# Performance work log

Hardware: AMD Instinct MI355X
Metric: run time of the kernel (lower is better)

## Reference

```python
import jax, jax.numpy as jnp
import numpy as np

B, N, P, E = 64, 512, 256, 4096          # batch, nodes (stations), partition nodes, edges
NUM_NWP, LP, F = 8, 16, 32               # num_nwp, local_points, local_cnn_dims
NT, ED, H, W = 8, 8, 64, 8               # num_temp, edge_feature_dims, decf_mlp_hidden, weight_function_dim
G, RH = 64, 256                          # gnn_dim, readout_hid_dim
H1, Q = 128, 9                           # mlp_hid_dim1, num quantiles


def setup_inputs() -> dict:
    key = jax.random.key(0)
    ks = iter(jax.random.split(key, 40))
    def rn(shape, s=0.05):
        return jax.random.normal(next(ks), shape, dtype=jnp.float32) * s
    # one-hot incidence matrices: each edge has one left (partition) node and one right node
    lidx = jax.random.randint(next(ks), (E,), 0, P)
    ridx = jax.random.randint(next(ks), (E,), 0, N)
    linc = jnp.zeros((P, E), jnp.float32).at[lidx, jnp.arange(E)].set(1.0)
    rinc = jnp.zeros((E, N), jnp.float32).at[jnp.arange(E), ridx].set(1.0)
    inp = {
        "x1": jax.random.normal(next(ks), (B, NUM_NWP * N, LP), dtype=jnp.float32),
        "x2": jax.random.normal(next(ks), (B, NT), dtype=jnp.float32),
        # LocalConv1D grouped conv (torch OIW layout: [Cout, Cin/groups, K])
        "conv_w": rn((F * N, NUM_NWP, LP)), "conv_b": rn((F * N,)),
        # WDSGCN2 edge-weight MLP
        "k1_w": rn((H, ED)), "k1_b": rn((H,)),
        "k2_w": rn((H, NT)),
        "k3_w": rn((H, F)),
        "k4_w": rn((H, F)),
        "k5_w": rn((W, H)), "k5_b": rn((W,)),
        "gc_w": rn((G, F * W)), "gc_b": rn((G,)),
        # readout
        "r0_w": rn((RH, G * P)),
        "r1_w": rn((RH, NT)), "r1_b": rn((RH,)),
        "r2_w": rn((RH, P)),
        "r3_w": rn((P, RH)), "r3_b": rn((P,)),
        # SMlp (forward uses l1 -> ELU -> l3 only)
        "l1_w": rn((H1, NT + G)), "l1_b": rn((H1,)),
        "l3_w": rn((Q, H1)), "l3_b": rn((Q,)),
        # buffers
        "ef": jax.random.normal(next(ks), (E, ED + 1), dtype=jnp.float32),
        "linc": linc,
        "rinc": rinc,
        "cap_feature": jax.random.normal(next(ks), (P,), dtype=jnp.float32),
        "partition_idx": jnp.arange(P, dtype=jnp.int32) * (N // P),
    }
    return inp


def reference(x1, x2, conv_w, conv_b, k1_w, k1_b, k2_w, k3_w, k4_w, k5_w, k5_b,
              gc_w, gc_b, r0_w, r1_w, r1_b, r2_w, r3_w, r3_b,
              l1_w, l1_b, l3_w, l3_b, ef, linc, rinc, cap_feature, partition_idx):
    b = x1.shape[0]
    # --- LocalConv1D: grouped conv1d (valid padding, output length 1) + ReLU ---
    y = jax.lax.conv_general_dilated(x1, conv_w, (1,), 'VALID',
                                     dimension_numbers=('NCH', 'OIH', 'NCH'),
                                     feature_group_count=N)
    x = jax.nn.relu(y + conv_b[None, :, None]).reshape(b, N, F)      # [B,N,F]
    # --- WDSGCN2: per-edge weight kernel ---
    kern = ef[:, :-1] @ k1_w.T + k1_b                                # [E,H]
    kern = kern[None] + (x2 @ k2_w.T)[:, None, :]                    # [B,E,H]
    xp = x[:, partition_idx, :]                                      # [B,P,F]
    kern = kern + jnp.einsum('pe,bpf->bef', linc, xp) @ k3_w.T       # left-node feats
    rx = jnp.einsum('en,bnf->bef', rinc, x)                          # right-node feats [B,E,F]
    kern = kern + rx @ k4_w.T
    kern = jax.nn.relu(jax.nn.leaky_relu(kern, 0.02) @ k5_w.T + k5_b)  # [B,E,W]
    # --- message = kernel (outer) right-node features, aggregated by left incidence ---
    msg = kern[:, :, :, None] * rx[:, :, None, :]                    # [B,E,W,F]
    agg = jnp.einsum('pe,bewf->bpwf', linc, msg).reshape(b, P, W * F)
    yg = jax.nn.relu(agg @ gc_w.T + gc_b)                            # [B,P,G]
    # --- readout attention over partition nodes ---
    h = yg.reshape(b, -1) @ r0_w.T + (x2 @ r1_w.T + r1_b) + cap_feature @ r2_w.T
    wt = jax.nn.relu(jax.nn.leaky_relu(h, 0.01) @ r3_w.T + r3_b)     # [B,P]
    res = jnp.einsum('bp,bpg->bg', wt, yg)                           # [B,G]
    # --- SMlp head ---
    z = jnp.concatenate([res, x2], axis=1)
    z = jax.nn.elu(z @ l1_w.T + l1_b)
    return z @ l3_w.T + l3_b                                         # [B,Q]
```

## Files before the change

kernel.cpp:

```cpp
#include <hip/hip_runtime.h>
#include <math.h>

#define B_ 64
#define N_ 512
#define P_ 256
#define E_ 4096
#define F_ 32
#define H_ 64
#define W_ 8
#define G_ 64
#define RH_ 256

#define X_OFF   0
#define T4_OFF  (X_OFF + N_*B_*F_)
#define T3_OFF  (T4_OFF + N_*B_*H_)
#define KB_OFF  (T3_OFF + P_*B_*H_)
#define KW_OFF  (KB_OFF + E_*H_)
#define YG_OFF  (KW_OFF + E_*B_*W_)
#define HB_OFF  (YG_OFF + B_*P_*G_)
#define RES_OFF (HB_OFF + B_*RH_)
#define INT_OFF (RES_OFF + 4*B_*G_)

__global__ __launch_bounds__(256) void k_decode(const float* __restrict__ linc,
    const float* __restrict__ rinc, int* __restrict__ lidx, int* __restrict__ ridx) {
  int i4 = blockIdx.x * 256 + threadIdx.x;
  const int L4 = (P_ * E_) / 4;
  if (i4 < L4) {
    float4 v = ((const float4*)linc)[i4];
    int i = i4 * 4;
    int p = i >> 12, e = i & 4095;
    if (v.x != 0.0f) lidx[e]     = p;
    if (v.y != 0.0f) lidx[e + 1] = p;
    if (v.z != 0.0f) lidx[e + 2] = p;
    if (v.w != 0.0f) lidx[e + 3] = p;
  } else {
    int j4 = i4 - L4;
    float4 v = ((const float4*)rinc)[j4];
    int j = j4 * 4;
    int e = j >> 9, n = j & 511;
    if (v.x != 0.0f) ridx[e] = n;
    if (v.y != 0.0f) ridx[e] = n + 1;
    if (v.z != 0.0f) ridx[e] = n + 2;
    if (v.w != 0.0f) ridx[e] = n + 3;
  }
}

__global__ __launch_bounds__(1024) void k_lists(const int* __restrict__ lidx,
    int* __restrict__ part_start, int* __restrict__ part_edges) {
  __shared__ int cnt[256];
  __shared__ int buf[256];
  __shared__ int cur[256];
  int t = threadIdx.x;
  if (t < 256) cnt[t] = 0;
  __syncthreads();
  for (int e = t; e < E_; e += 1024) atomicAdd(&cnt[lidx[e]], 1);
  __syncthreads();
  if (t < 256) buf[t] = cnt[t];
  __syncthreads();
  for (int off = 1; off < 256; off <<= 1) {
    int add = 0;
    if (t < 256 && t >= off) add = buf[t - off];
    __syncthreads();
    if (t < 256) buf[t] += add;
    __syncthreads();
  }
  if (t < 256) {
    part_start[t + 1] = buf[t];
    if (t == 0) part_start[0] = 0;
    cur[t] = buf[t] - cnt[t];
  }
  __syncthreads();
  for (int e = t; e < E_; e += 1024) {
    int p = lidx[e];
    int pos = atomicAdd(&cur[p], 1);
    part_edges[pos] = e;
  }
}

__global__ __launch_bounds__(256) void k_conv(const float* __restrict__ x1,
    const float* __restrict__ conv_w, const float* __restrict__ conv_b,
    float* __restrict__ x) {
  __shared__ float wsm[32 * 132];
  __shared__ float xsm[8192];
  int n = blockIdx.x, t = threadIdx.x;
  for (int i = t; i < 1024; i += 256) {
    int f = i >> 5, j = i & 31;
    ((float4*)wsm)[f * 33 + j] = ((const float4*)(conv_w + n * 4096))[i];
  }
  for (int i = t; i < 2048; i += 256) {
    int b = i >> 5, j = i & 31;
    ((float4*)xsm)[i] = ((const float4*)(x1 + b * 65536 + n * 128))[j];
  }
  __syncthreads();
  int f = t & 31, bq = t >> 5;
  float cb = conv_b[n * 32 + f];
  float acc[8];
#pragma unroll
  for (int bi = 0; bi < 8; bi++) acc[bi] = cb;
  const float4* wf4 = (const float4*)wsm + f * 33;
  const float4* xb4 = (const float4*)xsm + bq * 256;
#pragma unroll 4
  for (int k4 = 0; k4 < 32; k4++) {
    float4 wv = wf4[k4];
#pragma unroll
    for (int bi = 0; bi < 8; bi++) {
      float4 xv = xb4[bi * 32 + k4];
      acc[bi] += wv.x * xv.x + wv.y * xv.y + wv.z * xv.z + wv.w * xv.w;
    }
  }
#pragma unroll
  for (int bi = 0; bi < 8; bi++) {
    int b = bq * 8 + bi;
    x[n * 2048 + b * 32 + f] = fmaxf(acc[bi], 0.0f);
  }
}

__global__ __launch_bounds__(256) void k_prep(
    const float* __restrict__ x, const int* __restrict__ pidx,
    const float* __restrict__ k3_w, const float* __restrict__ k4_w,
    const float* __restrict__ x2, const float* __restrict__ k2_w,
    const float* __restrict__ ef, const float* __restrict__ k1_w,
    const float* __restrict__ k1_b,
    const float* __restrict__ r1_w, const float* __restrict__ r1_b,
    const float* __restrict__ r2_w, const float* __restrict__ cap,
    float* __restrict__ t4, float* __restrict__ t3, float* __restrict__ kb,
    float* __restrict__ hbuf) {
  __shared__ float xsh[2048];
  __shared__ float wsh[64 * 36];
  __shared__ float x2s[512];
  __shared__ float k2s[512];
  int blk = blockIdx.x, t = threadIdx.x;
  if (blk < 768) {
    bool isT4 = blk < 512;
    int n = isT4 ? blk : pidx[blk - 512];
    const float* wmat = isT4 ? k4_w : k3_w;
    float* outp = isT4 ? (t4 + blk * 4096) : (t3 + (blk - 512) * 4096);
    for (int i = t; i < 512; i += 256) {
      ((float4*)xsh)[i] = ((const float4*)(x + n * 2048))[i];
      int h = i >> 3, j = i & 7;
      ((float4*)wsh)[h * 9 + j] = ((const float4*)wmat)[i];
    }
    if (isT4) {
      for (int i = t; i < 128; i += 256) {
        ((float4*)x2s)[i] = ((const float4*)x2)[i];
        ((float4*)k2s)[i] = ((const float4*)k2_w)[i];
      }
    }
    __syncthreads();
    int h = t & 63, bq = t >> 6;
    float wreg[32];
#pragma unroll
    for (int j = 0; j < 8; j++) {
      float4 v = ((float4*)wsh)[h * 9 + j];
      wreg[4 * j] = v.x; wreg[4 * j + 1] = v.y; wreg[4 * j + 2] = v.z; wreg[4 * j + 3] = v.w;
    }
    float w2[8];
    if (isT4) {
      float4 u = ((float4*)k2s)[h * 2], v = ((float4*)k2s)[h * 2 + 1];
      w2[0] = u.x; w2[1] = u.y; w2[2] = u.z; w2[3] = u.w;
      w2[4] = v.x; w2[5] = v.y; w2[6] = v.z; w2[7] = v.w;
    }
    for (int bi = 0; bi < 16; bi++) {
      int b = bq * 16 + bi;
      float acc = 0.0f;
#pragma unroll
      for (int j = 0; j < 8; j++) {
        float4 xv = ((float4*)xsh)[b * 8 + j];
        acc += xv.x * wreg[4 * j] + xv.y * wreg[4 * j + 1] +
               xv.z * wreg[4 * j + 2] + xv.w * wreg[4 * j + 3];
      }
      if (isT4) {
        float4 u = ((float4*)x2s)[b * 2], v = ((float4*)x2s)[b * 2 + 1];
        acc += u.x * w2[0] + u.y * w2[1] + u.z * w2[2] + u.w * w2[3] +
               v.x * w2[4] + v.y * w2[5] + v.z * w2[6] + v.w * w2[7];
      }
      outp[b * 64 + h] = acc;
    }
  } else if (blk < 1792) {
    int o = (blk - 768) * 256 + t;
    int e = o >> 6, h = o & 63;
    float acc = k1_b[h];
    const float* er = ef + e * 9;
    const float* kr = k1_w + h * 8;
#pragma unroll
    for (int d = 0; d < 8; d++) acc += er[d] * kr[d];
    kb[o] = acc;
  } else {
    int o = (blk - 1792) * 256 + t;
    int rh = o & 255;
    float acc = r1_b[rh];
    const float* xr = x2 + (o >> 8) * 8;
    const float* rr = r1_w + rh * 8;
#pragma unroll
    for (int d = 0; d < 8; d++) acc += xr[d] * rr[d];
    const float* r2r = r2_w + rh * 256;
    for (int p4 = 0; p4 < 64; p4++) {
      float4 cv = ((const float4*)cap)[p4];
      float4 rv = ((const float4*)r2r)[p4];
      acc += cv.x * rv.x + cv.y * rv.y + cv.z * rv.z + cv.w * rv.w;
    }
    hbuf[o] = acc;
  }
}

__global__ __launch_bounds__(256) void k_edge(
    const float* __restrict__ kb, const float* __restrict__ t3,
    const float* __restrict__ t4, const float* __restrict__ k5_w,
    const float* __restrict__ k5_b, const int* __restrict__ lidx,
    const int* __restrict__ ridx, float* __restrict__ kw) {
  __shared__ float k5t[4 * 520];
  int e = blockIdx.x, t = threadIdx.x;
  for (int i = t; i < 512; i += 256) {
    int h = i >> 3, w = i & 7;
    float v = k5_w[w * 64 + h];
#pragma unroll
    for (int qq = 0; qq < 4; qq++) k5t[qq * 520 + i] = v;
  }
  int p = lidx[e], r = ridx[e];
  int q = t & 3, b = t >> 2;
  const float4* kb4 = (const float4*)(kb + e * 64 + q * 16);
  const float4* t34 = (const float4*)(t3 + p * 4096 + b * 64 + q * 16);
  const float4* t44 = (const float4*)(t4 + r * 4096 + b * 64 + q * 16);
  __syncthreads();
  float lk[16];
#pragma unroll
  for (int j4 = 0; j4 < 4; j4++) {
    float4 a = kb4[j4], c = t34[j4], d = t44[j4];
    float v;
    v = a.x + c.x + d.x; lk[j4 * 4 + 0] = v > 0.0f ? v : 0.02f * v;
    v = a.y + c.y + d.y; lk[j4 * 4 + 1] = v > 0.0f ? v : 0.02f * v;
    v = a.z + c.z + d.z; lk[j4 * 4 + 2] = v > 0.0f ? v : 0.02f * v;
    v = a.w + c.w + d.w; lk[j4 * 4 + 3] = v > 0.0f ? v : 0.02f * v;
  }
  float pw[8] = {0, 0, 0, 0, 0, 0, 0, 0};
  const float* kq = k5t + q * 520 + q * 128;
#pragma unroll
  for (int j = 0; j < 16; j++) {
    float4 u = *(const float4*)(kq + j * 8);
    float4 v = *(const float4*)(kq + j * 8 + 4);
    float l = lk[j];
    pw[0] += l * u.x; pw[1] += l * u.y; pw[2] += l * u.z; pw[3] += l * u.w;
    pw[4] += l * v.x; pw[5] += l * v.y; pw[6] += l * v.z; pw[7] += l * v.w;
  }
#pragma unroll
  for (int w = 0; w < 8; w++) {
    pw[w] += __shfl_xor(pw[w], 1);
    pw[w] += __shfl_xor(pw[w], 2);
  }
  float2 o;
  o.x = fmaxf(pw[2 * q] + k5_b[2 * q], 0.0f);
  o.y = fmaxf(pw[2 * q + 1] + k5_b[2 * q + 1], 0.0f);
  *(float2*)(kw + e * 512 + t * 2) = o;
}

__global__ __launch_bounds__(256) void k_agg_gc(const float* __restrict__ x,
    const float* __restrict__ kw, const int* __restrict__ ridx,
    const int* __restrict__ part_start, const int* __restrict__ part_edges,
    const float* __restrict__ gc_w, const float* __restrict__ gc_b,
    float* __restrict__ yg) {
  __shared__ unsigned short accS[64 * 256];
  int p = blockIdx.x, t = threadIdx.x;
  int b = t >> 2, s = t & 3;
  float acc[64];
#pragma unroll
  for (int j = 0; j < 64; j++) acc[j] = 0.0f;
  int s0 = part_start[p], s1 = part_start[p + 1];
  int idx = s0;
  for (; idx + 1 < s1; idx += 2) {
    int e0 = part_edges[idx], e1 = part_edges[idx + 1];
    int r0 = ridx[e0], r1 = ridx[e1];
    float2 ka = *(const float2*)(kw + e0 * 512 + b * 8 + s * 2);
    float2 kc = *(const float2*)(kw + e1 * 512 + b * 8 + s * 2);
    const float4* xp0 = (const float4*)(x + r0 * 2048 + b * 32);
    const float4* xp1 = (const float4*)(x + r1 * 2048 + b * 32);
    float xa[32], xb[32];
#pragma unroll
    for (int i = 0; i < 8; i++) {
      float4 v = xp0[i];
      xa[4 * i] = v.x; xa[4 * i + 1] = v.y; xa[4 * i + 2] = v.z; xa[4 * i + 3] = v.w;
    }
#pragma unroll
    for (int i = 0; i < 8; i++) {
      float4 v = xp1[i];
      xb[4 * i] = v.x; xb[4 * i + 1] = v.y; xb[4 * i + 2] = v.z; xb[4 * i + 3] = v.w;
    }
#pragma unroll
    for (int j = 0; j < 32; j++) acc[j] += ka.x * xa[j];
#pragma unroll
    for (int j = 0; j < 32; j++) acc[32 + j] += ka.y * xa[j];
#pragma unroll
    for (int j = 0; j < 32; j++) acc[j] += kc.x * xb[j];
#pragma unroll
    for (int j = 0; j < 32; j++) acc[32 + j] += kc.y * xb[j];
  }
  if (idx < s1) {
    int e0 = part_edges[idx];
    int r0 = ridx[e0];
    float2 ka = *(const float2*)(kw + e0 * 512 + b * 8 + s * 2);
    const float4* xp0 = (const float4*)(x + r0 * 2048 + b * 32);
    float xa[32];
#pragma unroll
    for (int i = 0; i < 8; i++) {
      float4 v = xp0[i];
      xa[4 * i] = v.x; xa[4 * i + 1] = v.y; xa[4 * i + 2] = v.z; xa[4 * i + 3] = v.w;
    }
#pragma unroll
    for (int j = 0; j < 32; j++) acc[j] += ka.x * xa[j];
#pragma unroll
    for (int j = 0; j < 32; j++) acc[32 + j] += ka.y * xa[j];
  }
#pragma unroll
  for (int o = 0; o < 8; o++) {
    int koct = s * 8 + o;
    int os = koct ^ (b >> 3);
    unsigned int wds[4];
#pragma unroll
    for (int h = 0; h < 4; h++) {
      unsigned int u0 = __float_as_uint(acc[o * 8 + 2 * h]);
      u0 = u0 + 0x7fffu + ((u0 >> 16) & 1u);
      unsigned int u1 = __float_as_uint(acc[o * 8 + 2 * h + 1]);
      u1 = u1 + 0x7fffu + ((u1 >> 16) & 1u);
      wds[h] = (u0 >> 16) | (u1 & 0xffff0000u);
    }
    int4 pk = make_int4((int)wds[0], (int)wds[1], (int)wds[2], (int)wds[3]);
    *(int4*)(accS + b * 256 + os * 8) = pk;
  }
  __syncthreads();
  int lane = t & 63, wv = t >> 6;
  int bg = lane >> 3, gg = lane & 7;
  int g0 = wv * 16 + gg * 2;
  const float* gw0 = gc_w + g0 * 256;
  const float* gw1 = gc_w + (g0 + 1) * 256;
  float ac[8][2];
#pragma unroll
  for (int i = 0; i < 8; i++) { ac[i][0] = 0.0f; ac[i][1] = 0.0f; }
  for (int oct = 0; oct < 32; oct++) {
    int4 a8[8];
#pragma unroll
    for (int i = 0; i < 8; i++) {
      int row = bg * 8 + i;
      int os = oct ^ bg;
      a8[i] = *(const int4*)(accS + row * 256 + os * 8);
    }
    float4 b0a = *(const float4*)(gw0 + oct * 8);
    float4 b0b = *(const float4*)(gw0 + oct * 8 + 4);
    float4 b1a = *(const float4*)(gw1 + oct * 8);
    float4 b1b = *(const float4*)(gw1 + oct * 8 + 4);
    float bv0[8] = {b0a.x, b0a.y, b0a.z, b0a.w, b0b.x, b0b.y, b0b.z, b0b.w};
    float bv1[8] = {b1a.x, b1a.y, b1a.z, b1a.w, b1b.x, b1b.y, b1b.z, b1b.w};
#pragma unroll
    for (int kk = 0; kk < 8; kk++) {
#pragma unroll
      for (int i = 0; i < 8; i++) {
        int w32;
        switch (kk >> 1) {
          case 0: w32 = a8[i].x; break;
          case 1: w32 = a8[i].y; break;
          case 2: w32 = a8[i].z; break;
          default: w32 = a8[i].w; break;
        }
        unsigned int u = (unsigned int)w32;
        unsigned int bits = (kk & 1) ? (u & 0xffff0000u) : (u << 16);
        float av = __uint_as_float(bits);
        ac[i][0] += av * bv0[kk];
        ac[i][1] += av * bv1[kk];
      }
    }
  }
  float gb0 = gc_b[g0], gb1 = gc_b[g0 + 1];
#pragma unroll
  for (int i = 0; i < 8; i++) {
    int bb = bg * 8 + i;
    float* yp = yg + bb * 16384 + p * 64;
    yp[g0]     = fmaxf(ac[i][0] + gb0, 0.0f);
    yp[g0 + 1] = fmaxf(ac[i][1] + gb1, 0.0f);
  }
}

__global__ __launch_bounds__(256) void k_r0(const float* __restrict__ yg,
    const float* __restrict__ r0_w, float* __restrict__ hbuf) {
  __shared__ float ygs[64 * 68];
  __shared__ float r0s[32 * 68];
  int blk = blockIdx.x;
  int rt = blk >> 6, kc = blk & 63;
  int t = threadIdx.x;
  int bg = t & 15, rg = t >> 4;
  float acc[4][2];
#pragma unroll
  for (int bi = 0; bi < 4; bi++)
#pragma unroll
    for (int ri = 0; ri < 2; ri++) acc[bi][ri] = 0.0f;
  for (int ks = 0; ks < 4; ks++) {
    int kbase = kc * 256 + ks * 64;
    __syncthreads();
    for (int i = t; i < 1024; i += 256) {
      int b = i >> 4, j = i & 15;
      ((float4*)ygs)[b * 17 + j] = *((const float4*)(yg + b * 16384 + kbase) + j);
    }
    for (int i = t; i < 512; i += 256) {
      int r = i >> 4, j = i & 15;
      ((float4*)r0s)[r * 17 + j] = *((const float4*)(r0_w + (rt * 32 + r) * 16384 + kbase) + j);
    }
    __syncthreads();
#pragma unroll 4
    for (int k4 = 0; k4 < 16; k4++) {
      float4 yv[4], rv[2];
#pragma unroll
      for (int bi = 0; bi < 4; bi++) yv[bi] = ((float4*)ygs)[(bg * 4 + bi) * 17 + k4];
#pragma unroll
      for (int ri = 0; ri < 2; ri++) rv[ri] = ((float4*)r0s)[(rg * 2 + ri) * 17 + k4];
#pragma unroll
      for (int bi = 0; bi < 4; bi++)
#pragma unroll
        for (int ri = 0; ri < 2; ri++)
          acc[bi][ri] += yv[bi].x * rv[ri].x + yv[bi].y * rv[ri].y +
                         yv[bi].z * rv[ri].z + yv[bi].w * rv[ri].w;
    }
  }
#pragma unroll
  for (int bi = 0; bi < 4; bi++)
#pragma unroll
    for (int ri = 0; ri < 2; ri++)
      atomicAdd(&hbuf[(bg * 4 + bi) * 256 + rt * 32 + rg * 2 + ri], acc[bi][ri]);
}

__global__ __launch_bounds__(256) void k_wt_res(const float* __restrict__ hbuf,
    const float* __restrict__ r3_w, const float* __restrict__ r3_b,
    const float* __restrict__ yg, float* __restrict__ res4) {
  __shared__ float hs[256];
  __shared__ float wts[64];
  __shared__ float red[256];
  int blk = blockIdx.x;
  int bb = blk >> 2, pq = blk & 3;
  int t = threadIdx.x;
  float hv = hbuf[bb * 256 + t];
  hs[t] = hv > 0.0f ? hv : 0.01f * hv;
  __syncthreads();
  int pl = t >> 2, c = t & 3;
  int pp = pq * 64 + pl;
  const float4* wrow = (const float4*)(r3_w + pp * 256 + c * 64);
  const float4* h4 = (const float4*)(hs) + c * 16;
  float a = 0.0f;
#pragma unroll
  for (int j = 0; j < 16; j++) {
    float4 w4 = wrow[j], hh = h4[j];
    a += hh.x * w4.x + hh.y * w4.y + hh.z * w4.z + hh.w * w4.w;
  }
  a += __shfl_xor(a, 1);
  a += __shfl_xor(a, 2);
  if (c == 0) wts[pl] = fmaxf(a + r3_b[pp], 0.0f);
  __syncthreads();
  int g = t & 63, ch = t >> 6;
  float r = 0.0f;
  const float* ygp = yg + bb * 16384 + pq * 4096 + g;
#pragma unroll
  for (int pi = 0; pi < 16; pi++) {
    int pl2 = ch * 16 + pi;
    r += wts[pl2] * ygp[pl2 * 64];
  }
  red[t] = r;
  __syncthreads();
  if (t < 64)
    res4[pq * 4096 + bb * 64 + t] = red[t] + red[t + 64] + red[t + 128] + red[t + 192];
}

__global__ __launch_bounds__(128) void k_final(const float* __restrict__ res4,
    const float* __restrict__ x2, const float* __restrict__ l1_w,
    const float* __restrict__ l1_b, const float* __restrict__ l3_w,
    const float* __restrict__ l3_b, float* __restrict__ out) {
  __shared__ float zs[128];
  int bb = blockIdx.x, t = threadIdx.x;
  float acc = l1_b[t];
  const float* wrow = l1_w + t * 72;
  const float* rr = res4 + bb * 64;
#pragma unroll 8
  for (int j = 0; j < 64; j++) {
    float rv = rr[j] + rr[4096 + j] + rr[8192 + j] + rr[12288 + j];
    acc += rv * wrow[j];
  }
  const float* xr = x2 + bb * 8;
#pragma unroll
  for (int j = 0; j < 8; j++) acc += xr[j] * wrow[64 + j];
  zs[t] = acc > 0.0f ? acc : expm1f(acc);
  __syncthreads();
  if (t < 9) {
    float o = l3_b[t];
    const float* w3 = l3_w + t * 128;
    for (int j = 0; j < 128; j++) o += zs[j] * w3[j];
    out[bb * 9 + t] = o;
  }
}

extern "C" void kernel_launch(void* const* d_in, const int* in_sizes, int n_in,
                              void* d_out, int out_size, void* d_ws, size_t ws_size,
                              hipStream_t stream) {
  (void)in_sizes; (void)n_in; (void)out_size; (void)ws_size;
  const float* x1     = (const float*)d_in[0];
  const float* x2     = (const float*)d_in[1];
  const float* conv_w = (const float*)d_in[2];
  const float* conv_b = (const float*)d_in[3];
  const float* k1_w   = (const float*)d_in[4];
  const float* k1_b   = (const float*)d_in[5];
  const float* k2_w   = (const float*)d_in[6];
  const float* k3_w   = (const float*)d_in[7];
  const float* k4_w   = (const float*)d_in[8];
  const float* k5_w   = (const float*)d_in[9];
  const float* k5_b   = (const float*)d_in[10];
  const float* gc_w   = (const float*)d_in[11];
  const float* gc_b   = (const float*)d_in[12];
  const float* r0_w   = (const float*)d_in[13];
  const float* r1_w   = (const float*)d_in[14];
  const float* r1_b   = (const float*)d_in[15];
  const float* r2_w   = (const float*)d_in[16];
  const float* r3_w   = (const float*)d_in[17];
  const float* r3_b   = (const float*)d_in[18];
  const float* l1_w   = (const float*)d_in[19];
  const float* l1_b   = (const float*)d_in[20];
  const float* l3_w   = (const float*)d_in[21];
  const float* l3_b   = (const float*)d_in[22];
  const float* ef     = (const float*)d_in[23];
  const float* linc   = (const float*)d_in[24];
  const float* rinc   = (const float*)d_in[25];
  const float* cap    = (const float*)d_in[26];
  const int*   pidx   = (const int*)d_in[27];
  float* out = (float*)d_out;

  float* ws   = (float*)d_ws;
  float* xbuf = ws + X_OFF;
  float* t4   = ws + T4_OFF;
  float* t3   = ws + T3_OFF;
  float* kb   = ws + KB_OFF;
  float* kwb  = ws + KW_OFF;
  float* yg   = ws + YG_OFF;
  float* hbuf = ws + HB_OFF;
  float* res4 = ws + RES_OFF;
  int* ib = (int*)(ws + INT_OFF);
  int* lidx = ib;
  int* ridx = ib + 4096;
  int* part_start = ib + 8192;
  int* part_edges = ib + 8704;

  hipLaunchKernelGGL(k_decode, dim3(3072), dim3(256), 0, stream, linc, rinc, lidx, ridx);
  hipLaunchKernelGGL(k_lists, dim3(1), dim3(1024), 0, stream, lidx, part_start, part_edges);
  hipLaunchKernelGGL(k_conv, dim3(512), dim3(256), 0, stream, x1, conv_w, conv_b, xbuf);
  hipLaunchKernelGGL(k_prep, dim3(1856), dim3(256), 0, stream,
                     xbuf, pidx, k3_w, k4_w, x2, k2_w, ef, k1_w, k1_b,
                     r1_w, r1_b, r2_w, cap, t4, t3, kb, hbuf);
  hipLaunchKernelGGL(k_edge, dim3(4096), dim3(256), 0, stream,
                     kb, t3, t4, k5_w, k5_b, lidx, ridx, kwb);
  hipLaunchKernelGGL(k_agg_gc, dim3(256), dim3(256), 0, stream,
                     xbuf, kwb, ridx, part_start, part_edges, gc_w, gc_b, yg);
  hipLaunchKernelGGL(k_r0, dim3(512), dim3(256), 0, stream, yg, r0_w, hbuf);
  hipLaunchKernelGGL(k_wt_res, dim3(256), dim3(256), 0, stream, hbuf, r3_w, r3_b, yg, res4);
  hipLaunchKernelGGL(k_final, dim3(64), dim3(128), 0, stream,
                     res4, x2, l1_w, l1_b, l3_w, l3_b, out);
}
```

Baseline: 273.2 us.

## Retile r0 GEMM as split-K with register blocking, batch edges per block

After: 264.4 us. 3.2% less time.

```diff
diff --git a/kernel.cpp b/kernel.cpp
--- a/kernel.cpp
+++ b/kernel.cpp
@@ -209,48 +209,52 @@
     const float* __restrict__ k5_b, const int* __restrict__ lidx,
     const int* __restrict__ ridx, float* __restrict__ kw) {
   __shared__ float k5t[4 * 520];
-  int e = blockIdx.x, t = threadIdx.x;
+  int e0 = blockIdx.x * 4, t = threadIdx.x;
   for (int i = t; i < 512; i += 256) {
     int h = i >> 3, w = i & 7;
     float v = k5_w[w * 64 + h];
 #pragma unroll
     for (int qq = 0; qq < 4; qq++) k5t[qq * 520 + i] = v;
   }
-  int p = lidx[e], r = ridx[e];
   int q = t & 3, b = t >> 2;
-  const float4* kb4 = (const float4*)(kb + e * 64 + q * 16);
-  const float4* t34 = (const float4*)(t3 + p * 4096 + b * 64 + q * 16);
-  const float4* t44 = (const float4*)(t4 + r * 4096 + b * 64 + q * 16);
-  __syncthreads();
-  float lk[16];
-#pragma unroll
-  for (int j4 = 0; j4 < 4; j4++) {
-    float4 a = kb4[j4], c = t34[j4], d = t44[j4];
-    float v;
-    v = a.x + c.x + d.x; lk[j4 * 4 + 0] = v > 0.0f ? v : 0.02f * v;
-    v = a.y + c.y + d.y; lk[j4 * 4 + 1] = v > 0.0f ? v : 0.02f * v;
-    v = a.z + c.z + d.z; lk[j4 * 4 + 2] = v > 0.0f ? v : 0.02f * v;
-    v = a.w + c.w + d.w; lk[j4 * 4 + 3] = v > 0.0f ? v : 0.02f * v;
-  }
-  float pw[8] = {0, 0, 0, 0, 0, 0, 0, 0};
   const float* kq = k5t + q * 520 + q * 128;
-#pragma unroll
-  for (int j = 0; j < 16; j++) {
-    float4 u = *(const float4*)(kq + j * 8);
-    float4 v = *(const float4*)(kq + j * 8 + 4);
-    float l = lk[j];
-    pw[0] += l * u.x; pw[1] += l * u.y; pw[2] += l * u.z; pw[3] += l * u.w;
-    pw[4] += l * v.x; pw[5] += l * v.y; pw[6] += l * v.z; pw[7] += l * v.w;
-  }
-#pragma unroll
-  for (int w = 0; w < 8; w++) {
-    pw[w] += __shfl_xor(pw[w], 1);
-    pw[w] += __shfl_xor(pw[w], 2);
-  }
-  float2 o;
-  o.x = fmaxf(pw[2 * q] + k5_b[2 * q], 0.0f);
-  o.y = fmaxf(pw[2 * q + 1] + k5_b[2 * q + 1], 0.0f);
-  *(float2*)(kw + e * 512 + t * 2) = o;
+  float kb5_0 = k5_b[2 * q], kb5_1 = k5_b[2 * q + 1];
+  __syncthreads();
+  for (int ei = 0; ei < 4; ei++) {
+    int e = e0 + ei;
+    int p = lidx[e], r = ridx[e];
+    const float4* kb4 = (const float4*)(kb + e * 64 + q * 16);
+    const float4* t34 = (const float4*)(t3 + p * 4096 + b * 64 + q * 16);
+    const float4* t44 = (const float4*)(t4 + r * 4096 + b * 64 + q * 16);
+    float lk[16];
+#pragma unroll
+    for (int j4 = 0; j4 < 4; j4++) {
+      float4 a = kb4[j4], c = t34[j4], d = t44[j4];
+      float v;
+      v = a.x + c.x + d.x; lk[j4 * 4 + 0] = v > 0.0f ? v : 0.02f * v;
+      v = a.y + c.y + d.y; lk[j4 * 4 + 1] = v > 0.0f ? v : 0.02f * v;
+      v = a.z + c.z + d.z; lk[j4 * 4 + 2] = v > 0.0f ? v : 0.02f * v;
+      v = a.w + c.w + d.w; lk[j4 * 4 + 3] = v > 0.0f ? v : 0.02f * v;
+    }
+    float pw[8] = {0, 0, 0, 0, 0, 0, 0, 0};
+#pragma unroll
+    for (int j = 0; j < 16; j++) {
+      float4 u = *(const float4*)(kq + j * 8);
+      float4 v = *(const float4*)(kq + j * 8 + 4);
+      float l = lk[j];
+      pw[0] += l * u.x; pw[1] += l * u.y; pw[2] += l * u.z; pw[3] += l * u.w;
+      pw[4] += l * v.x; pw[5] += l * v.y; pw[6] += l * v.z; pw[7] += l * v.w;
+    }
+#pragma unroll
+    for (int w = 0; w < 8; w++) {
+      pw[w] += __shfl_xor(pw[w], 1);
+      pw[w] += __shfl_xor(pw[w], 2);
+    }
+    float2 o;
+    o.x = fmaxf(pw[2 * q] + kb5_0, 0.0f);
+    o.y = fmaxf(pw[2 * q + 1] + kb5_1, 0.0f);
+    *(float2*)(kw + e * 512 + t * 2) = o;
+  }
 }
 
 __global__ __launch_bounds__(256) void k_agg_gc(const float* __restrict__ x,
@@ -378,50 +382,79 @@
 }
 
 __global__ __launch_bounds__(256) void k_r0(const float* __restrict__ yg,
-    const float* __restrict__ r0_w, float* __restrict__ hbuf) {
+    const float* __restrict__ r0_w, float* __restrict__ part) {
   __shared__ float ygs[64 * 68];
-  __shared__ float r0s[32 * 68];
+  __shared__ float wts[64 * 260];
+  int kc = blockIdx.x, t = threadIdx.x;
+  int k0 = kc * 64;
+  {
+    int rr = t >> 4, c = t & 15;
+    for (int rd = 0; rd < 16; rd++) {
+      int rh = rd * 16 + rr;
+      float4 v = *(const float4*)(r0_w + rh * 16384 + k0 + c * 4);
+      wts[(4 * c + 0) * 260 + rh] = v.x;
+      wts[(4 * c + 1) * 260 + rh] = v.y;
+      wts[(4 * c + 2) * 260 + rh] = v.z;
+      wts[(4 * c + 3) * 260 + rh] = v.w;
+    }
+  }
+  {
+    int b = t >> 2, kq = t & 3;
+    const float* src = yg + b * 16384 + k0 + kq * 16;
+#pragma unroll
+    for (int u = 0; u < 4; u++) {
+      float4 v = *(const float4*)(src + u * 4);
+      int kk = kq * 16 + u * 4;
+      ygs[(kk + 0) * 68 + b] = v.x;
+      ygs[(kk + 1) * 68 + b] = v.y;
+      ygs[(kk + 2) * 68 + b] = v.z;
+      ygs[(kk + 3) * 68 + b] = v.w;
+    }
+  }
+  __syncthreads();
+  int lane = t & 63, wv = t >> 6;
+  int b8 = lane & 7, r8 = lane >> 3;
+  const float* yp = ygs + b8 * 8;
+  const float* wp = wts + wv * 64 + r8 * 8;
+  float acc[8][8];
+#pragma unroll
+  for (int i = 0; i < 8; i++)
+#pragma unroll
+    for (int j = 0; j < 8; j++) acc[i][j] = 0.0f;
+#pragma unroll 2
+  for (int k = 0; k < 64; k++) {
+    float4 ya = *(const float4*)(yp + k * 68);
+    float4 yb = *(const float4*)(yp + k * 68 + 4);
+    float4 wa = *(const float4*)(wp + k * 260);
+    float4 wb = *(const float4*)(wp + k * 260 + 4);
+    float yv[8] = {ya.x, ya.y, ya.z, ya.w, yb.x, yb.y, yb.z, yb.w};
+    float wr[8] = {wa.x, wa.y, wa.z, wa.w, wb.x, wb.y, wb.z, wb.w};
+#pragma unroll
+    for (int i = 0; i < 8; i++)
+#pragma unroll
+      for (int j = 0; j < 8; j++) acc[i][j] += yv[i] * wr[j];
+  }
+  float* pb = part + kc * 16384 + wv * 64 + r8 * 8;
+#pragma unroll
+  for (int i = 0; i < 8; i++) {
+    float4 s0 = make_float4(acc[i][0], acc[i][1], acc[i][2], acc[i][3]);
+    float4 s1 = make_float4(acc[i][4], acc[i][5], acc[i][6], acc[i][7]);
+    float* pp = pb + (b8 * 8 + i) * 256;
+    *(float4*)pp = s0;
+    *(float4*)(pp + 4) = s1;
+  }
+}
+
+__global__ __launch_bounds__(256) void k_r0red(const float* __restrict__ part,
+    float* __restrict__ hbuf) {
   int blk = blockIdx.x;
-  int rt = blk >> 6, kc = blk & 63;
-  int t = threadIdx.x;
-  int bg = t & 15, rg = t >> 4;
-  float acc[4][2];
-#pragma unroll
-  for (int bi = 0; bi < 4; bi++)
-#pragma unroll
-    for (int ri = 0; ri < 2; ri++) acc[bi][ri] = 0.0f;
-  for (int ks = 0; ks < 4; ks++) {
-    int kbase = kc * 256 + ks * 64;
-    __syncthreads();
-    for (int i = t; i < 1024; i += 256) {
-      int b = i >> 4, j = i & 15;
-      ((float4*)ygs)[b * 17 + j] = *((const float4*)(yg + b * 16384 + kbase) + j);
-    }
-    for (int i = t; i < 512; i += 256) {
-      int r = i >> 4, j = i & 15;
-      ((float4*)r0s)[r * 17 + j] = *((const float4*)(r0_w + (rt * 32 + r) * 16384 + kbase) + j);
-    }
-    __syncthreads();
-#pragma unroll 4
-    for (int k4 = 0; k4 < 16; k4++) {
-      float4 yv[4], rv[2];
-#pragma unroll
-      for (int bi = 0; bi < 4; bi++) yv[bi] = ((float4*)ygs)[(bg * 4 + bi) * 17 + k4];
-#pragma unroll
-      for (int ri = 0; ri < 2; ri++) rv[ri] = ((float4*)r0s)[(rg * 2 + ri) * 17 + k4];
-#pragma unroll
-      for (int bi = 0; bi < 4; bi++)
-#pragma unroll
-        for (int ri = 0; ri < 2; ri++)
-          acc[bi][ri] += yv[bi].x * rv[ri].x + yv[bi].y * rv[ri].y +
-                         yv[bi].z * rv[ri].z + yv[bi].w * rv[ri].w;
-    }
-  }
-#pragma unroll
-  for (int bi = 0; bi < 4; bi++)
-#pragma unroll
-    for (int ri = 0; ri < 2; ri++)
-      atomicAdd(&hbuf[(bg * 4 + bi) * 256 + rt * 32 + rg * 2 + ri], acc[bi][ri]);
+  int oq = blk & 63, kq = blk >> 6;
+  int o = oq * 256 + threadIdx.x;
+  float s = 0.0f;
+  const float* pp = part + kq * 64 * 16384 + o;
+#pragma unroll 8
+  for (int kc = 0; kc < 64; kc++) s += pp[kc * 16384];
+  atomicAdd(&hbuf[o], s);
 }
 
 __global__ __launch_bounds__(256) void k_wt_res(const float* __restrict__ hbuf,
@@ -534,6 +567,7 @@
   float* yg   = ws + YG_OFF;
   float* hbuf = ws + HB_OFF;
   float* res4 = ws + RES_OFF;
+  float* part = ws + X_OFF;
   int* ib = (int*)(ws + INT_OFF);
   int* lidx = ib;
   int* ridx = ib + 4096;
@@ -546,11 +580,12 @@
   hipLaunchKernelGGL(k_prep, dim3(1856), dim3(256), 0, stream,
                      xbuf, pidx, k3_w, k4_w, x2, k2_w, ef, k1_w, k1_b,
                      r1_w, r1_b, r2_w, cap, t4, t3, kb, hbuf);
-  hipLaunchKernelGGL(k_edge, dim3(4096), dim3(256), 0, stream,
+  hipLaunchKernelGGL(k_edge, dim3(1024), dim3(256), 0, stream,
                      kb, t3, t4, k5_w, k5_b, lidx, ridx, kwb);
   hipLaunchKernelGGL(k_agg_gc, dim3(256), dim3(256), 0, stream,
                      xbuf, kwb, ridx, part_start, part_edges, gc_w, gc_b, yg);
-  hipLaunchKernelGGL(k_r0, dim3(512), dim3(256), 0, stream, yg, r0_w, hbuf);
+  hipLaunchKernelGGL(k_r0, dim3(256), dim3(256), 0, stream, yg, r0_w, part);
+  hipLaunchKernelGGL(k_r0red, dim3(256), dim3(256), 0, stream, part, hbuf);
   hipLaunchKernelGGL(k_wt_res, dim3(256), dim3(256), 0, stream, hbuf, r3_w, r3_b, yg, res4);
   hipLaunchKernelGGL(k_final, dim3(64), dim3(128), 0, stream,
                      res4, x2, l1_w, l1_b, l3_w, l3_b, out);
```
